# Kernel tuning notes

Measured on AMD Instinct MI355X. Metric: run time of the kernel, lower is better.

## Reference

```python
import jax, jax.numpy as jnp
import numpy as np

N = 50000      # nodes
E = 500000     # edges
IN = 128       # in_channels
HID = 64       # hidden_channels
OUT = 128      # out_channels
H = 4          # heads
NEG_SLOPE = 0.2


def _glorot(key, shape):
    fan_in, fan_out = shape[0], shape[-1]
    lim = np.sqrt(6.0 / (fan_in + fan_out))
    return jax.random.uniform(key, shape, jnp.float32, -lim, lim)


def setup_inputs() -> dict:
    key = jax.random.key(0)
    ks = jax.random.split(key, 12)
    return {
        "x": jax.random.normal(ks[0], (N, IN), jnp.float32),
        "edge_index": jax.random.randint(ks[1], (2, E), 0, N, jnp.int64),
        "edge_weight": jax.random.uniform(ks[2], (E,), jnp.float32),
        # layer 1: IN -> H*HID
        "W1": _glorot(ks[3], (IN, H * HID)),
        "b1": jnp.zeros((H * HID,), jnp.float32),
        "att1": _glorot(ks[4], (H, HID)),
        # layer 2: HID -> H*HID  (update() means over heads -> HID features)
        "W2": _glorot(ks[5], (HID, H * HID)),
        "b2": jnp.zeros((H * HID,), jnp.float32),
        "att2": _glorot(ks[6], (H, HID)),
        # layer 3: HID -> H*OUT
        "W3": _glorot(ks[7], (HID, H * OUT)),
        "b3": jnp.zeros((H * OUT,), jnp.float32),
        "att3": _glorot(ks[8], (H, OUT)),
    }


def _gat_layer(x, W, b, att, src, dst, edge_weight, out_dim):
    # lin + reshape to [N, H, D]
    h = (x @ W + b).reshape(-1, H, out_dim)
    xj = h[src]                                   # gather source feats [E,H,D]
    alpha = jnp.sum(xj * att[None], axis=-1)      # per-edge att score [E,H]
    alpha = jax.nn.leaky_relu(alpha, NEG_SLOPE)
    alpha = alpha * edge_weight[:, None]
    alpha = jax.nn.softmax(alpha, axis=1)         # softmax over HEADS (dim=1, as in source)
    msg = xj * alpha[:, :, None]                  # [E,H,D]
    aggr = jax.ops.segment_sum(msg, dst, num_segments=N)  # scatter-add [N,H,D]
    return aggr.mean(axis=1)                      # update(): mean over heads -> [N,D]


def reference(x, edge_index, edge_weight, W1, b1, att1, W2, b2, att2, W3, b3, att3):
    src, dst = edge_index[0], edge_index[1]
    h = _gat_layer(x, W1, b1, att1, src, dst, edge_weight, HID)
    h = jax.nn.relu(h)
    h = _gat_layer(h, W2, b2, att2, src, dst, edge_weight, HID)
    h = jax.nn.relu(h)
    return _gat_layer(h, W3, b3, att3, src, dst, edge_weight, OUT)
```

## Files before the change

### kernel.cpp

```cpp
#include <hip/hip_runtime.h>
#include <hip/hip_bf16.h>

#define NHEAD 4
#define NEG 0.2f

typedef __bf16 bf16x8 __attribute__((ext_vector_type(8)));
typedef __bf16 bf16x4 __attribute__((ext_vector_type(4)));
typedef float f32x4 __attribute__((ext_vector_type(4)));

__device__ __forceinline__ float blo(unsigned u) { return __uint_as_float(u << 16); }
__device__ __forceinline__ float bhi(unsigned u) { return __uint_as_float(u & 0xffff0000u); }
__device__ __forceinline__ unsigned short fbits(float f) {
    __bf16 h = (__bf16)f;
    return *(unsigned short*)&h;
}


__global__ __launch_bounds__(256) void hist_k(const int* __restrict__ dst,
                                              int* __restrict__ deg, int E) {
    int e = blockIdx.x * 256 + threadIdx.x;
    if (e < E) atomicAdd(&deg[dst[e]], 1);
}

__global__ __launch_bounds__(256) void partial_k(const int* __restrict__ deg,
                                                 int* __restrict__ bsum, int n) {
    int t = threadIdx.x;
    int base = blockIdx.x * 2048 + t * 8;
    int s = 0;
#pragma unroll
    for (int i = 0; i < 8; ++i) {
        int idx = base + i;
        if (idx < n) s += deg[idx];
    }
#pragma unroll
    for (int off = 32; off; off >>= 1) s += __shfl_down(s, off, 64);
    __shared__ int ws[4];
    if ((t & 63) == 0) ws[t >> 6] = s;
    __syncthreads();
    if (t == 0) bsum[blockIdx.x] = ws[0] + ws[1] + ws[2] + ws[3];
}

__global__ __launch_bounds__(256) void bscan_k(const int* __restrict__ bsum,
                                               int* __restrict__ boff, int nb) {
    __shared__ int sh[256];
    int t = threadIdx.x;
    int v = (t < nb) ? bsum[t] : 0;
    sh[t] = v;
    __syncthreads();
    for (int off = 1; off < 256; off <<= 1) {
        int u = (t >= off) ? sh[t - off] : 0;
        __syncthreads();
        sh[t] += u;
        __syncthreads();
    }
    if (t < nb) boff[t] = sh[t] - v;
}

__global__ __launch_bounds__(256) void rescan_k(const int* __restrict__ deg,
                                                const int* __restrict__ boff,
                                                int* __restrict__ rowptr,
                                                int* __restrict__ fill,
                                                int n, int total) {
    __shared__ int ts[256];
    int t = threadIdx.x;
    int base = blockIdx.x * 2048 + t * 8;
    int v[8];
    int s = 0;
#pragma unroll
    for (int i = 0; i < 8; ++i) {
        int idx = base + i;
        v[i] = (idx < n) ? deg[idx] : 0;
        s += v[i];
    }
    ts[t] = s;
    __syncthreads();
    for (int off = 1; off < 256; off <<= 1) {
        int u = (t >= off) ? ts[t - off] : 0;
        __syncthreads();
        ts[t] += u;
        __syncthreads();
    }
    int run = boff[blockIdx.x] + ts[t] - s;
#pragma unroll
    for (int i = 0; i < 8; ++i) {
        int idx = base + i;
        if (idx < n) {
            rowptr[idx] = run;
            fill[idx] = run;
            run += v[i];
        }
    }
    if (blockIdx.x == 0 && t == 0) rowptr[n] = total;
}

__global__ __launch_bounds__(256) void scatter_k(const int* __restrict__ src,
                                                 const int* __restrict__ dst,
                                                 const float* __restrict__ ew,
                                                 int* __restrict__ fill,
                                                 int* __restrict__ srcs,
                                                 float* __restrict__ wsrt, int E) {
    int e = blockIdx.x * 256 + threadIdx.x;
    if (e < E) {
        int d = dst[e];
        int p = atomicAdd(&fill[d], 1);
        srcs[p] = src[e];
        wsrt[p] = ew[e];
    }
}


__global__ __launch_bounds__(256) void prep_k(const float* __restrict__ W1, const float* __restrict__ att1, const float* __restrict__ b1,
                                              const float* __restrict__ W2, const float* __restrict__ att2, const float* __restrict__ b2,
                                              const float* __restrict__ W3, const float* __restrict__ att3, const float* __restrict__ b3,
                                              float* __restrict__ v1, float* __restrict__ v2, float* __restrict__ v3,
                                              float* __restrict__ c1, float* __restrict__ c2, float* __restrict__ c3) {
    int tid = blockIdx.x * 256 + threadIdx.x;
    if (tid < 512) {
        int h = tid >> 7, k = tid & 127;
        float p = 0.f;
        for (int d = 0; d < 64; ++d) p += W1[k * 256 + h * 64 + d] * att1[h * 64 + d];
        v1[h * 128 + k] = p;
    } else if (tid < 768) {
        int t = tid - 512, h = t >> 6, k = t & 63;
        float p = 0.f;
        for (int d = 0; d < 64; ++d) p += W2[k * 256 + h * 64 + d] * att2[h * 64 + d];
        v2[h * 64 + k] = p;
    } else if (tid < 1024) {
        int t = tid - 768, h = t >> 6, k = t & 63;
        float p = 0.f;
        for (int d = 0; d < 128; ++d) p += W3[k * 512 + h * 128 + d] * att3[h * 128 + d];
        v3[h * 64 + k] = p;
    } else if (tid < 1028) {
        int h = tid - 1024;
        float p = 0.f;
        for (int d = 0; d < 64; ++d) p += b1[h * 64 + d] * att1[h * 64 + d];
        c1[h] = p;
    } else if (tid < 1032) {
        int h = tid - 1028;
        float p = 0.f;
        for (int d = 0; d < 64; ++d) p += b2[h * 64 + d] * att2[h * 64 + d];
        c2[h] = p;
    } else if (tid < 1036) {
        int h = tid - 1032;
        float p = 0.f;
        for (int d = 0; d < 128; ++d) p += b3[h * 128 + d] * att3[h * 128 + d];
        c3[h] = p;
    }
}


__global__ __launch_bounds__(256) void wpack3_k(const float* __restrict__ W1,
                                                const float* __restrict__ W2,
                                                const float* __restrict__ W3,
                                                unsigned short* __restrict__ Ws1,
                                                unsigned short* __restrict__ Ws2,
                                                unsigned short* __restrict__ Ws3) {
    int tid = blockIdx.x * 256 + threadIdx.x;
    if (tid < 32768) {
        int d = tid >> 9, r = tid & 511, h = r >> 7, k = r & 127;
        Ws1[tid] = fbits(W1[k * 256 + h * 64 + d]);
    } else if (tid < 49152) {
        int t = tid - 32768;
        int d = t >> 8, r = t & 255, h = r >> 6, k = r & 63;
        Ws2[t] = fbits(W2[k * 256 + h * 64 + d]);
    } else if (tid < 81920) {
        int t = tid - 49152;
        int d = t >> 8, r = t & 255, h = r >> 6, k = r & 63;
        Ws3[t] = fbits(W3[k * 512 + h * 128 + d]);
    }
}


__global__ __launch_bounds__(256) void xpack_score_k(const float* __restrict__ x,
                                                     const float* __restrict__ v1,
                                                     const float* __restrict__ c1,
                                                     unsigned* __restrict__ xb,
                                                     float* __restrict__ s, int n) {
    int gt = blockIdx.x * 256 + threadIdx.x;
    int node = gt >> 6, lane = gt & 63;
    if (node >= n) return;
    float2 xv = ((const float2*)(x + (size_t)node * 128))[lane];
    xb[(size_t)node * 64 + lane] = (unsigned)fbits(xv.x) | ((unsigned)fbits(xv.y) << 16);
    int d0 = 2 * lane;
    float p0 = xv.x * v1[0 * 128 + d0] + xv.y * v1[0 * 128 + d0 + 1];
    float p1 = xv.x * v1[1 * 128 + d0] + xv.y * v1[1 * 128 + d0 + 1];
    float p2 = xv.x * v1[2 * 128 + d0] + xv.y * v1[2 * 128 + d0 + 1];
    float p3 = xv.x * v1[3 * 128 + d0] + xv.y * v1[3 * 128 + d0 + 1];
#pragma unroll
    for (int off = 32; off; off >>= 1) {
        p0 += __shfl_xor(p0, off, 64);
        p1 += __shfl_xor(p1, off, 64);
        p2 += __shfl_xor(p2, off, 64);
        p3 += __shfl_xor(p3, off, 64);
    }
    if (lane == 0)
        *(float4*)&s[(size_t)node * 4] = make_float4(p0 + c1[0], p1 + c1[1], p2 + c1[2], p3 + c1[3]);
}


__device__ __forceinline__ float4 edge_alpha(const float* __restrict__ s, int sn, float w) {
    float4 sv = *(const float4*)&s[(size_t)sn * 4];
    float a0 = (sv.x > 0.f ? sv.x : NEG * sv.x) * w;
    float a1 = (sv.y > 0.f ? sv.y : NEG * sv.y) * w;
    float a2 = (sv.z > 0.f ? sv.z : NEG * sv.z) * w;
    float a3 = (sv.w > 0.f ? sv.w : NEG * sv.w) * w;
    float m = fmaxf(fmaxf(a0, a1), fmaxf(a2, a3));
    float e0 = __expf(a0 - m), e1 = __expf(a1 - m);
    float e2 = __expf(a2 - m), e3 = __expf(a3 - m);
    float inv = 0.25f / (e0 + e1 + e2 + e3);
    return make_float4(e0 * inv, e1 * inv, e2 * inv, e3 * inv);
}


template <int K, int D, bool LAST>
__global__ __launch_bounds__(256, 4) void fused_k(const int* __restrict__ rowptr,
                                                  const int* __restrict__ srcs,
                                                  const float* __restrict__ wsrt,
                                                  const float* __restrict__ sprev,
                                                  const unsigned* __restrict__ xb,
                                                  const unsigned short* __restrict__ Ws,
                                                  const float* __restrict__ bias,
                                                  const float* __restrict__ vnext,
                                                  const float* __restrict__ cnext,
                                                  unsigned short* __restrict__ aout,
                                                  float* __restrict__ fout,
                                                  float* __restrict__ snext,
                                                  int n) {
    constexpr int HK = 4 * K;
    constexpr int KS = HK / 32;
    constexpr int NC = D / 16;
    constexpr int CW = NC / 4;
    constexpr int DW = K / 32;

    __shared__ __bf16 gh[16 * HK];
    __shared__ __bf16 gl[16 * HK];
    __shared__ float4 A_lds[16];
    __shared__ float4 sc_lds[4][16];

    int t = threadIdx.x;
    int r0 = blockIdx.x * 16;
    int n4 = t >> 4, sl = t & 15;
    int node = r0 + n4;

    float acc[4][2 * DW];
#pragma unroll
    for (int h = 0; h < 4; ++h)
#pragma unroll
        for (int j = 0; j < 2 * DW; ++j) acc[h][j] = 0.f;
    float4 aA = make_float4(0.f, 0.f, 0.f, 0.f);

    auto load_u = [&](int sn, unsigned* u) {
        if constexpr (DW == 4) {
            uint4 ta = ((const uint4*)xb)[(size_t)sn * 16 + sl];
            u[0] = ta.x; u[1] = ta.y; u[2] = ta.z; u[3] = ta.w;
        } else {
            uint2 ta = ((const uint2*)xb)[(size_t)sn * 16 + sl];
            u[0] = ta.x; u[1] = ta.y;
        }
    };
    auto accum = [&](float4 al, const unsigned* u) {
#pragma unroll
        for (int j = 0; j < DW; ++j) {
            float x0 = blo(u[j]), x1 = bhi(u[j]);
            acc[0][2 * j] += al.x * x0; acc[0][2 * j + 1] += al.x * x1;
            acc[1][2 * j] += al.y * x0; acc[1][2 * j + 1] += al.y * x1;
            acc[2][2 * j] += al.z * x0; acc[2][2 * j + 1] += al.z * x1;
            acc[3][2 * j] += al.w * x0; acc[3][2 * j + 1] += al.w * x1;
        }
        aA.x += al.x; aA.y += al.y; aA.z += al.z; aA.w += al.w;
    };

    if (node < n) {
        int beg = rowptr[node], end = rowptr[node + 1];
        int e = beg;
        for (; e + 3 < end; e += 4) {
            int sn0 = srcs[e], sn1 = srcs[e + 1], sn2 = srcs[e + 2], sn3 = srcs[e + 3];
            float w0 = wsrt[e], w1 = wsrt[e + 1], w2 = wsrt[e + 2], w3 = wsrt[e + 3];
            unsigned u0[DW], u1[DW], u2[DW], u3[DW];
            load_u(sn0, u0); load_u(sn1, u1); load_u(sn2, u2); load_u(sn3, u3);
            float4 al0 = edge_alpha(sprev, sn0, w0);
            float4 al1 = edge_alpha(sprev, sn1, w1);
            float4 al2 = edge_alpha(sprev, sn2, w2);
            float4 al3 = edge_alpha(sprev, sn3, w3);
            accum(al0, u0); accum(al1, u1); accum(al2, u2); accum(al3, u3);
        }
        for (; e < end; ++e) {
            int sn = srcs[e];
            unsigned u[DW];
            load_u(sn, u);
            float4 al = edge_alpha(sprev, sn, wsrt[e]);
            accum(al, u);
        }
    }

    {
        char* ghb = (char*)gh + (size_t)n4 * (HK * 2);
        char* glb = (char*)gl + (size_t)n4 * (HK * 2);
        int sw = (n4 & 7) << 4;
#pragma unroll
        for (int h = 0; h < 4; ++h) {
            if constexpr (DW == 4) {
                bf16x8 vh, vl;
#pragma unroll
                for (int j = 0; j < 8; ++j) {
                    __bf16 hi = (__bf16)acc[h][j];
                    vh[j] = hi;
                    vl[j] = (__bf16)(acc[h][j] - (float)hi);
                }
                int bo = (h * K + sl * 8) * 2;
                *(bf16x8*)(ghb + (bo ^ sw)) = vh;
                *(bf16x8*)(glb + (bo ^ sw)) = vl;
            } else {
                bf16x4 vh, vl;
#pragma unroll
                for (int j = 0; j < 4; ++j) {
                    __bf16 hi = (__bf16)acc[h][j];
                    vh[j] = hi;
                    vl[j] = (__bf16)(acc[h][j] - (float)hi);
                }
                int bo = (h * K + sl * 4) * 2;
                *(bf16x4*)(ghb + (bo ^ sw)) = vh;
                *(bf16x4*)(glb + (bo ^ sw)) = vl;
            }
        }
        if (sl == 0) A_lds[n4] = aA;
    }
    __syncthreads();

    int wid = t >> 6, lane = t & 63;
    int lrow = lane & 15, gq = lane >> 4;

    f32x4 acc2[CW];
#pragma unroll
    for (int cw = 0; cw < CW; ++cw)
#pragma unroll
        for (int r = 0; r < 4; ++r) acc2[cw][r] = 0.f;

    const __bf16* wsp = (const __bf16*)Ws;
    const char* ghr = (const char*)gh + (size_t)lrow * (HK * 2);
    const char* glr = (const char*)gl + (size_t)lrow * (HK * 2);
    int swr = (lrow & 7) << 4;
#pragma unroll
    for (int ks = 0; ks < KS; ++ks) {
        int bo = ks * 64 + gq * 16;
        bf16x8 fh = *(const bf16x8*)(ghr + (bo ^ swr));
        bf16x8 fl = *(const bf16x8*)(glr + (bo ^ swr));
#pragma unroll
        for (int cw = 0; cw < CW; ++cw) {
            int c = wid * CW + cw;
            bf16x8 bfr = *(const bf16x8*)(wsp + (size_t)(c * 16 + lrow) * HK + ks * 32 + gq * 8);
            acc2[cw] = __builtin_amdgcn_mfma_f32_16x16x32_bf16(fh, bfr, acc2[cw], 0, 0, 0);
            acc2[cw] = __builtin_amdgcn_mfma_f32_16x16x32_bf16(fl, bfr, acc2[cw], 0, 0, 0);
        }
    }

    float4 Ar[4];
#pragma unroll
    for (int r = 0; r < 4; ++r) Ar[r] = A_lds[gq * 4 + r];

    float sc[4][4];
#pragma unroll
    for (int h = 0; h < 4; ++h)
#pragma unroll
        for (int r = 0; r < 4; ++r) sc[h][r] = 0.f;

#pragma unroll
    for (int cw = 0; cw < CW; ++cw) {
        int col = (wid * CW + cw) * 16 + lrow;
        float bb0 = bias[0 * D + col], bb1 = bias[1 * D + col];
        float bb2 = bias[2 * D + col], bb3 = bias[3 * D + col];
        float vv0 = 0.f, vv1 = 0.f, vv2 = 0.f, vv3 = 0.f;
        if constexpr (!LAST) {
            vv0 = vnext[0 * D + col]; vv1 = vnext[1 * D + col];
            vv2 = vnext[2 * D + col]; vv3 = vnext[3 * D + col];
        }
#pragma unroll
        for (int r = 0; r < 4; ++r) {
            float val = acc2[cw][r] + Ar[r].x * bb0 + Ar[r].y * bb1 + Ar[r].z * bb2 + Ar[r].w * bb3;
            int row = r0 + gq * 4 + r;
            if constexpr (LAST) {
                if (row < n) fout[(size_t)row * D + col] = val;
            } else {
                val = fmaxf(val, 0.f);
                if (row < n) aout[(size_t)row * D + col] = fbits(val);
                sc[0][r] += val * vv0;
                sc[1][r] += val * vv1;
                sc[2][r] += val * vv2;
                sc[3][r] += val * vv3;
            }
        }
    }

    if constexpr (!LAST) {
#pragma unroll
        for (int m = 1; m < 16; m <<= 1) {
#pragma unroll
            for (int h = 0; h < 4; ++h)
#pragma unroll
                for (int r = 0; r < 4; ++r) sc[h][r] += __shfl_xor(sc[h][r], m, 64);
        }
        if (lrow < 4) {
            int r = lrow;
            sc_lds[wid][gq * 4 + r] = make_float4(sc[0][r], sc[1][r], sc[2][r], sc[3][r]);
        }
        __syncthreads();
        if (t < 16) {
            int row = r0 + t;
            if (row < n) {
                float4 s0 = sc_lds[0][t], s1 = sc_lds[1][t];
                float4 s2 = sc_lds[2][t], s3 = sc_lds[3][t];
                *(float4*)&snext[(size_t)row * 4] =
                    make_float4(s0.x + s1.x + s2.x + s3.x + cnext[0],
                                s0.y + s1.y + s2.y + s3.y + cnext[1],
                                s0.z + s1.z + s2.z + s3.z + cnext[2],
                                s0.w + s1.w + s2.w + s3.w + cnext[3]);
            }
        }
    }
}


extern "C" void kernel_launch(void* const* d_in, const int* in_sizes, int n_in,
                              void* d_out, int out_size, void* d_ws, size_t ws_size,
                              hipStream_t stream) {
    const float* x    = (const float*)d_in[0];
    const int*   ei   = (const int*)d_in[1];
    const float* ew   = (const float*)d_in[2];
    const float* W1   = (const float*)d_in[3];
    const float* b1   = (const float*)d_in[4];
    const float* att1 = (const float*)d_in[5];
    const float* W2   = (const float*)d_in[6];
    const float* b2   = (const float*)d_in[7];
    const float* att2 = (const float*)d_in[8];
    const float* W3   = (const float*)d_in[9];
    const float* b3   = (const float*)d_in[10];
    const float* att3 = (const float*)d_in[11];

    const int N = in_sizes[0] / 128;
    const int E = in_sizes[2];
    const int* src = ei;
    const int* dst = ei + E;

    char* wp = (char*)d_ws;
    auto alloc = [&](size_t bytes) -> void* {
        void* p = (void*)wp;
        wp += (bytes + 511) & ~(size_t)511;
        return p;
    };
    int*   deg    = (int*)alloc((size_t)N * 4);
    int*   rowptr = (int*)alloc((size_t)(N + 1) * 4);
    int*   fill   = (int*)alloc((size_t)N * 4);
    int*   bsum   = (int*)alloc(256 * 4);
    int*   boff   = (int*)alloc(256 * 4);
    int*   srcs   = (int*)alloc((size_t)E * 4);
    float* wsrt   = (float*)alloc((size_t)E * 4);
    unsigned* xb  = (unsigned*)alloc((size_t)N * 64 * 4);
    float* s      = (float*)alloc((size_t)N * 4 * 4);
    float* s2     = (float*)alloc((size_t)N * 4 * 4);
    unsigned short* a1 = (unsigned short*)alloc((size_t)N * 64 * 2);
    unsigned short* a2 = (unsigned short*)alloc((size_t)N * 64 * 2);
    float* v1 = (float*)alloc(512 * 4);
    float* v2 = (float*)alloc(256 * 4);
    float* v3 = (float*)alloc(256 * 4);
    float* c1 = (float*)alloc(16);
    float* c2 = (float*)alloc(16);
    float* c3 = (float*)alloc(16);
    unsigned short* Ws1 = (unsigned short*)alloc(32768 * 2);
    unsigned short* Ws2 = (unsigned short*)alloc(16384 * 2);
    unsigned short* Ws3 = (unsigned short*)alloc(32768 * 2);

    wpack3_k<<<320, 256, 0, stream>>>(W1, W2, W3, Ws1, Ws2, Ws3);
    prep_k<<<5, 256, 0, stream>>>(W1, att1, b1, W2, att2, b2, W3, att3, b3,
                                  v1, v2, v3, c1, c2, c3);
    int gx = (N * 64 + 255) / 256;
    xpack_score_k<<<gx, 256, 0, stream>>>(x, v1, c1, xb, s, N);

    hipMemsetAsync(deg, 0, (size_t)N * 4, stream);
    int ge = (E + 255) / 256;
    int nb = (N + 2047) / 2048;
    hist_k<<<ge, 256, 0, stream>>>(dst, deg, E);
    partial_k<<<nb, 256, 0, stream>>>(deg, bsum, N);
    bscan_k<<<1, 256, 0, stream>>>(bsum, boff, nb);
    rescan_k<<<nb, 256, 0, stream>>>(deg, boff, rowptr, fill, N, E);
    scatter_k<<<ge, 256, 0, stream>>>(src, dst, ew, fill, srcs, wsrt, E);

    int gf = (N + 15) / 16;

    fused_k<128, 64, false><<<gf, 256, 0, stream>>>(rowptr, srcs, wsrt, s, xb, Ws1, b1,
                                                    v2, c2, a1, nullptr, s2, N);

    fused_k<64, 64, false><<<gf, 256, 0, stream>>>(rowptr, srcs, wsrt, s2, (const unsigned*)a1,
                                                   Ws2, b2, v3, c3, a2, nullptr, s, N);

    fused_k<64, 128, true><<<gf, 256, 0, stream>>>(rowptr, srcs, wsrt, s, (const unsigned*)a2,
                                                   Ws3, b3, nullptr, nullptr, nullptr,
                                                   (float*)d_out, nullptr, N);
}
```

Measured before the change: 257.1 us.

## Compute per-edge attention once per block into LDS instead of per lane

Previously each of the 16 lanes serving a node recomputed the per-edge softmax-over-heads coefficients, including a gather of the source score vector and four exps. Now the block cooperatively computes the coefficients for its contiguous edge range in chunks of 256, one edge per thread, and stores them in shared memory. The per-node gather loops then read the coefficients from LDS. The cost is two block-wide barriers per chunk plus load imbalance, since every thread waits for the whole chunk.

```diff
diff --git a/kernel.cpp b/kernel.cpp
--- a/kernel.cpp
+++ b/kernel.cpp
@@ -198,20 +198,6 @@
 }
 
 
-__device__ __forceinline__ float4 edge_alpha(const float* __restrict__ s, int sn, float w) {
-    float4 sv = *(const float4*)&s[(size_t)sn * 4];
-    float a0 = (sv.x > 0.f ? sv.x : NEG * sv.x) * w;
-    float a1 = (sv.y > 0.f ? sv.y : NEG * sv.y) * w;
-    float a2 = (sv.z > 0.f ? sv.z : NEG * sv.z) * w;
-    float a3 = (sv.w > 0.f ? sv.w : NEG * sv.w) * w;
-    float m = fmaxf(fmaxf(a0, a1), fmaxf(a2, a3));
-    float e0 = __expf(a0 - m), e1 = __expf(a1 - m);
-    float e2 = __expf(a2 - m), e3 = __expf(a3 - m);
-    float inv = 0.25f / (e0 + e1 + e2 + e3);
-    return make_float4(e0 * inv, e1 * inv, e2 * inv, e3 * inv);
-}
-
-
 template <int K, int D, bool LAST>
 __global__ __launch_bounds__(256, 4) void fused_k(const int* __restrict__ rowptr,
                                                   const int* __restrict__ srcs,
@@ -231,9 +217,11 @@
     constexpr int NC = D / 16;
     constexpr int CW = NC / 4;
     constexpr int DW = K / 32;
+    constexpr int CHUNK = 256;
 
     __shared__ __bf16 gh[16 * HK];
     __shared__ __bf16 gl[16 * HK];
+    __shared__ float4 al_lds[CHUNK];
     __shared__ float4 A_lds[16];
     __shared__ float4 sc_lds[4][16];
 
@@ -241,6 +229,13 @@
     int r0 = blockIdx.x * 16;
     int n4 = t >> 4, sl = t & 15;
     int node = r0 + n4;
+
+    int hi = min(r0 + 16, n);
+    int eb = rowptr[r0];
+    int ee = rowptr[hi];
+
+    int beg = 0, end = 0;
+    if (node < n) { beg = rowptr[node]; end = rowptr[node + 1]; }
 
     float acc[4][2 * DW];
 #pragma unroll
@@ -270,27 +265,47 @@
         aA.x += al.x; aA.y += al.y; aA.z += al.z; aA.w += al.w;
     };
 
-    if (node < n) {
-        int beg = rowptr[node], end = rowptr[node + 1];
-        int e = beg;
-        for (; e + 3 < end; e += 4) {
+    for (int cs = eb; cs < ee; cs += CHUNK) {
+        int ce = min(cs + CHUNK, ee);
+        {
+            int i = cs + t;
+            if (i < ce) {
+                int sn = srcs[i];
+                float w = wsrt[i];
+                float4 sv = *(const float4*)&sprev[(size_t)sn * 4];
+                float a0 = (sv.x > 0.f ? sv.x : NEG * sv.x) * w;
+                float a1 = (sv.y > 0.f ? sv.y : NEG * sv.y) * w;
+                float a2 = (sv.z > 0.f ? sv.z : NEG * sv.z) * w;
+                float a3 = (sv.w > 0.f ? sv.w : NEG * sv.w) * w;
+                float m = fmaxf(fmaxf(a0, a1), fmaxf(a2, a3));
+                float e0 = __expf(a0 - m), e1 = __expf(a1 - m);
+                float e2 = __expf(a2 - m), e3 = __expf(a3 - m);
+                float inv = 0.25f / (e0 + e1 + e2 + e3);
+                al_lds[i - cs] = make_float4(e0 * inv, e1 * inv, e2 * inv, e3 * inv);
+            }
+        }
+        __syncthreads();
+
+        int gb = max(beg, cs), ge = min(end, ce);
+        int e = gb;
+        for (; e + 3 < ge; e += 4) {
             int sn0 = srcs[e], sn1 = srcs[e + 1], sn2 = srcs[e + 2], sn3 = srcs[e + 3];
-            float w0 = wsrt[e], w1 = wsrt[e + 1], w2 = wsrt[e + 2], w3 = wsrt[e + 3];
             unsigned u0[DW], u1[DW], u2[DW], u3[DW];
             load_u(sn0, u0); load_u(sn1, u1); load_u(sn2, u2); load_u(sn3, u3);
-            float4 al0 = edge_alpha(sprev, sn0, w0);
-            float4 al1 = edge_alpha(sprev, sn1, w1);
-            float4 al2 = edge_alpha(sprev, sn2, w2);
-            float4 al3 = edge_alpha(sprev, sn3, w3);
+            float4 al0 = al_lds[e - cs];
+            float4 al1 = al_lds[e + 1 - cs];
+            float4 al2 = al_lds[e + 2 - cs];
+            float4 al3 = al_lds[e + 3 - cs];
             accum(al0, u0); accum(al1, u1); accum(al2, u2); accum(al3, u3);
         }
-        for (; e < end; ++e) {
+        for (; e < ge; ++e) {
             int sn = srcs[e];
             unsigned u[DW];
             load_u(sn, u);
-            float4 al = edge_alpha(sprev, sn, wsrt[e]);
+            float4 al = al_lds[e - cs];
             accum(al, u);
         }
+        __syncthreads();
     }
 
     {
@@ -303,9 +318,9 @@
                 bf16x8 vh, vl;
 #pragma unroll
                 for (int j = 0; j < 8; ++j) {
-                    __bf16 hi = (__bf16)acc[h][j];
-                    vh[j] = hi;
-                    vl[j] = (__bf16)(acc[h][j] - (float)hi);
+                    __bf16 hiw = (__bf16)acc[h][j];
+                    vh[j] = hiw;
+                    vl[j] = (__bf16)(acc[h][j] - (float)hiw);
                 }
                 int bo = (h * K + sl * 8) * 2;
                 *(bf16x8*)(ghb + (bo ^ sw)) = vh;
@@ -314,9 +329,9 @@
                 bf16x4 vh, vl;
 #pragma unroll
                 for (int j = 0; j < 4; ++j) {
-                    __bf16 hi = (__bf16)acc[h][j];
-                    vh[j] = hi;
-                    vl[j] = (__bf16)(acc[h][j] - (float)hi);
+                    __bf16 hiw = (__bf16)acc[h][j];
+                    vh[j] = hiw;
+                    vl[j] = (__bf16)(acc[h][j] - (float)hiw);
                 }
                 int bo = (h * K + sl * 4) * 2;
                 *(bf16x4*)(ghb + (bo ^ sw)) = vh;
```

Result: faster. 242.7 us (median of 2 runs) (-5.6%).
